# Performance work log

Hardware: AMD Instinct MI355X
Metric: run time of the kernel (lower is better)

## Reference

```python
import jax, jax.numpy as jnp
import numpy as np

N = 4096   # out_features (rows of W)
M = 4096   # in_features (cols of W)
S_L = 2048 # Givens pairs on rows
S_R = 2048 # Givens pairs on cols
T = 8192   # tokens (batch*seq)
EPS = 1e-6


def _disjoint_pairs(key, n_feat, n_pairs):
    perm = jax.random.permutation(key, n_feat)[: 2 * n_pairs]
    return perm.reshape(n_pairs, 2).astype(jnp.int32)


def setup_inputs() -> dict:
    key = jax.random.key(0)
    ks = jax.random.split(key, 8)
    x = jax.random.normal(ks[0], (T, M), dtype=jnp.float32)
    W = 0.02 * jax.random.normal(ks[1], (N, M), dtype=jnp.float32)
    bias = jnp.zeros((N,), dtype=jnp.float32)
    theta_L = 0.002 * jax.random.normal(ks[2], (S_L,), dtype=jnp.float32)
    theta_R = 0.002 * jax.random.normal(ks[3], (S_R,), dtype=jnp.float32)
    pairs_L = _disjoint_pairs(ks[4], N, S_L)
    pairs_R = _disjoint_pairs(ks[5], M, S_R)
    ecd_log_mag = jnp.zeros((N,), dtype=jnp.float32)
    base_row_norms = jnp.linalg.norm(W, axis=1)  # [N], captured at init
    return {"x": x, "W": W, "bias": bias, "theta_L": theta_L,
            "theta_R": theta_R, "ecd_log_mag": ecd_log_mag,
            "base_row_norms": base_row_norms, "pairs_L": pairs_L,
            "pairs_R": pairs_R}


def _rotate_rows(Wm, pairs, theta):
    # Disjoint Givens rotations on rows: gather pair rows, 2x2 rotate, scatter.
    i, j = pairs[:, 0], pairs[:, 1]
    c = jnp.cos(theta)[:, None]
    s = jnp.sin(theta)[:, None]
    ri, rj = Wm[i], Wm[j]              # [S, M] gathers
    return Wm.at[i].set(c * ri - s * rj).at[j].set(s * ri + c * rj)


def _rotate_cols(Wm, pairs, theta):
    i, j = pairs[:, 0], pairs[:, 1]
    c = jnp.cos(theta)[None, :]
    s = jnp.sin(theta)[None, :]
    ci, cj = Wm[:, i], Wm[:, j]        # [N, S] gathers
    return Wm.at[:, i].set(c * ci - s * cj).at[:, j].set(s * ci + c * cj)


def reference(x, W, bias, theta_L, theta_R, ecd_log_mag, base_row_norms,
              pairs_L, pairs_R):
    # Effective weight: W_eff = G_L(theta_L) @ W @ G_R(theta_R)^T
    W_eff = _rotate_rows(_rotate_cols(W, pairs_R, theta_R), pairs_L, theta_L)
    # Magnitude (ECD) rescaling: restore base per-row norms modulated by
    # learned log-magnitudes.
    row_norms = jnp.sqrt(jnp.sum(W_eff * W_eff, axis=1) + EPS)  # [N]
    scale = base_row_norms * jnp.exp(ecd_log_mag) / row_norms   # [N]
    W_eff = W_eff * scale[:, None]
    return x @ W_eff.T + bias
```

## Files before the change

kernel.cpp:

```cpp
#include <hip/hip_runtime.h>
#include <cstdint>
#include <cstddef>

constexpr int T_N = 8192;
constexpr int MM  = 4096;
constexpr int NN  = 4096;
constexpr int S_L = 2048;
constexpr int S_R = 2048;
constexpr float EPS_ = 1e-6f;

typedef float  f32x4   __attribute__((ext_vector_type(4)));
typedef __bf16 bf16x8  __attribute__((ext_vector_type(8)));
typedef unsigned short ushort8 __attribute__((ext_vector_type(8)));

__device__ __forceinline__ unsigned short f2bf(float f) {
  unsigned int u = __float_as_uint(f);
  u += 0x7FFFu + ((u >> 16) & 1u);
  return (unsigned short)(u >> 16);
}

__global__ void init_cols(float* colC, float* colS, int* colP) {
  int i = blockIdx.x * blockDim.x + threadIdx.x;
  if (i < MM) { colC[i] = 1.f; colS[i] = 0.f; colP[i] = i; }
}

__global__ void build_cols(const float* __restrict__ thR, const int* __restrict__ prR,
                           float* colC, float* colS, int* colP) {
  int s = blockIdx.x * blockDim.x + threadIdx.x;
  if (s < S_R) {
    int i = prR[2*s], j = prR[2*s+1];
    float c = cosf(thR[s]), sn = sinf(thR[s]);
    colC[i] = c; colS[i] = -sn; colP[i] = j;
    colC[j] = c; colS[j] =  sn; colP[j] = i;
  }
}

__global__ __launch_bounds__(256) void weff_pair(
    const float* __restrict__ W, const float* __restrict__ brn, const float* __restrict__ elm,
    const float* __restrict__ thL, const int* __restrict__ prL,
    const float* __restrict__ colC, const float* __restrict__ colS, const int* __restrict__ colP,
    unsigned short* __restrict__ Wb)
{
  __shared__ __align__(16) float rI[MM];
  __shared__ __align__(16) float rJ[MM];
  __shared__ float red[8];

  int s   = blockIdx.x;
  int tid = threadIdx.x;
  int i = prL[2*s], j = prL[2*s+1];
  float cl = cosf(thL[s]), sl = sinf(thL[s]);
  const float* Wi = W + (size_t)i * MM;
  const float* Wj = W + (size_t)j * MM;

  for (int m = tid * 4; m < MM; m += 1024) {
    *(f32x4*)&rI[m] = *(const f32x4*)&Wi[m];
    *(f32x4*)&rJ[m] = *(const f32x4*)&Wj[m];
  }
  __syncthreads();

  float ssi = 0.f, ssj = 0.f;
  for (int m = tid; m < MM; m += 256) {
    int p = colP[m];
    float c = colC[m], sn = colS[m];
    float vi = c * rI[m] + sn * rI[p];
    float vj = c * rJ[m] + sn * rJ[p];
    float ei = cl * vi - sl * vj;
    float ej = sl * vi + cl * vj;
    ssi += ei * ei;
    ssj += ej * ej;
  }
  #pragma unroll
  for (int o = 32; o; o >>= 1) { ssi += __shfl_xor(ssi, o); ssj += __shfl_xor(ssj, o); }
  int lane = tid & 63, wid = tid >> 6;
  if (lane == 0) { red[wid] = ssi; red[4 + wid] = ssj; }
  __syncthreads();
  float ti = red[0] + red[1] + red[2] + red[3];
  float tj = red[4] + red[5] + red[6] + red[7];
  float sci = brn[i] * expf(elm[i]) / sqrtf(ti + EPS_);
  float scj = brn[j] * expf(elm[j]) / sqrtf(tj + EPS_);

  for (int m0 = tid * 8; m0 < MM; m0 += 2048) {
    ushort8 pi, pj;
    #pragma unroll
    for (int q = 0; q < 8; q++) {
      int m = m0 + q;
      int p = colP[m];
      float c = colC[m], sn = colS[m];
      float vi = c * rI[m] + sn * rI[p];
      float vj = c * rJ[m] + sn * rJ[p];
      pi[q] = f2bf((cl * vi - sl * vj) * sci);
      pj[q] = f2bf((sl * vi + cl * vj) * scj);
    }
    *(ushort8*)&Wb[(size_t)i * MM + m0] = pi;
    *(ushort8*)&Wb[(size_t)j * MM + m0] = pj;
  }
}

__global__ __launch_bounds__(256) void conv_x(const float* __restrict__ x,
                                              unsigned short* __restrict__ xb) {
  const size_t total = (size_t)T_N * MM / 8;
  for (size_t i = (size_t)blockIdx.x * 256 + threadIdx.x; i < total; i += 2048ull * 256ull) {
    const float* s = x + i * 8;
    f32x4 v0 = *(const f32x4*)s;
    f32x4 v1 = *(const f32x4*)(s + 4);
    ushort8 p;
    p[0] = f2bf(v0.x); p[1] = f2bf(v0.y); p[2] = f2bf(v0.z); p[3] = f2bf(v0.w);
    p[4] = f2bf(v1.x); p[5] = f2bf(v1.y); p[6] = f2bf(v1.z); p[7] = f2bf(v1.w);
    *(ushort8*)(xb + i * 8) = p;
  }
}

typedef const __attribute__((address_space(1))) unsigned int* as1_u32p;
typedef __attribute__((address_space(3))) unsigned int* as3_u32p;

__device__ __forceinline__ void gl_lds16(const void* g, void* l) {
  __builtin_amdgcn_global_load_lds((as1_u32p)g, (as3_u32p)l, 16, 0, 0);
}

constexpr int GBM = 256, GBN = 256, GBK = 64;
constexpr int NTK = MM / GBK;
constexpr int BUFB = GBM * GBK * 2;

#define SB0() __builtin_amdgcn_sched_barrier(0)
#define BAR() __builtin_amdgcn_s_barrier()
#define LGKM(N) do { asm volatile("s_waitcnt lgkmcnt(" #N ")" ::: "memory"); \
                     SB0(); } while (0)

#define RD_A8(DST, AB, MIH)                                                   \
  _Pragma("unroll") for (int i_ = 0; i_ < 4; ++i_)                            \
  _Pragma("unroll") for (int k_ = 0; k_ < 2; ++k_)                            \
    DST[i_][k_] = *(const bf16x8*)((AB) + arow0 + ((MIH) * 4 + i_) * 2048     \
                                    + ((k_ * 64 + lg * 16) ^ sw));

#define RD_B4(DST, BB, NIH)                                                   \
  _Pragma("unroll") for (int n_ = 0; n_ < 2; ++n_)                            \
  _Pragma("unroll") for (int k_ = 0; k_ < 2; ++k_)                            \
    DST[n_][k_] = *(const bf16x8*)((BB) + brow0 + ((NIH) * 2 + n_) * 2048     \
                                    + ((k_ * 64 + lg * 16) ^ sw));

#define QMF(AF, BF, MI0, NI0)                                                 \
  __builtin_amdgcn_s_setprio(1);                                              \
  _Pragma("unroll") for (int k_ = 0; k_ < 2; ++k_)                            \
  _Pragma("unroll") for (int i_ = 0; i_ < 4; ++i_)                            \
  _Pragma("unroll") for (int n_ = 0; n_ < 2; ++n_)                            \
    acc[(MI0) + i_][(NI0) + n_] = __builtin_amdgcn_mfma_f32_16x16x32_bf16(    \
        AF[i_][k_], BF[n_][k_], acc[(MI0) + i_][(NI0) + n_], 0, 0, 0);        \
  __builtin_amdgcn_s_setprio(0);

#define STG_A(KOF, BUF, H)                                                    \
  _Pragma("unroll") for (int l_ = 2 * (H); l_ < 2 * (H) + 2; ++l_)            \
    gl_lds16(sA + (size_t)l_ * (64 * MM) + (KOF),                             \
             ldsA + (BUF) * BUFB + dstb + l_ * 8192);
#define STG_B(KOF, BUF, H)                                                    \
  _Pragma("unroll") for (int l_ = 2 * (H); l_ < 2 * (H) + 2; ++l_)            \
    gl_lds16(sB + (size_t)l_ * (64 * MM) + (KOF),                             \
             ldsB + (BUF) * BUFB + dstb + l_ * 8192);

#define GATE6  asm volatile("s_waitcnt vmcnt(6)" ::: "memory")
#define GATE0v asm volatile("s_waitcnt vmcnt(0)" ::: "memory")
#define GNONE  do { } while (0)

#define TILE8(T, BB, DOB1, DOA2, GATEK)                                       \
  {                                                                           \
    const char* Ab_ = ldsA + (BB) * BUFB;                                     \
    const char* Bb_ = ldsB + (BB) * BUFB;                                     \
    bf16x8 afA[4][2], afB[4][2], bfA[2][2], bfB[2][2];                        \
           \
    RD_A8(afA, Ab_, 0);                                                       \
    RD_B4(bfA, Bb_, 0);                                                       \
    if (DOB1) { STG_B(((T) + 1) * GBK, (BB) ^ 1, 1); }                        \
    LGKM(8);                                                                  \
    BAR();                                                                    \
    LGKM(0);                                                                  \
    QMF(afA, bfA, 0, 0);                                                      \
    BAR();                                                                    \
                                         \
    RD_A8(afB, Ab_, 1);                                                       \
    BAR();                                                                    \
    LGKM(0);                                                                  \
    QMF(afB, bfA, 4, 0);                                                      \
    BAR();                                                                    \
                          \
    RD_B4(bfB, Bb_, 1);                                                       \
    if (DOA2) { STG_A(((T) + 2) * GBK, (BB), 0); }                            \
    BAR();                                                                    \
    LGKM(0);                                                                  \
    QMF(afB, bfB, 4, 2);                                                      \
    BAR();                                                                    \
               \
    if (DOA2) { STG_A(((T) + 2) * GBK, (BB), 1);                              \
                STG_B(((T) + 2) * GBK, (BB), 0); }                            \
    GATEK;                                                                    \
    BAR();                                                                    \
    QMF(afA, bfB, 0, 2);                                                      \
    BAR();                                                                    \
  }

__global__ __launch_bounds__(512, 2) void gemm8(
    const unsigned short* __restrict__ xb,
    const unsigned short* __restrict__ wb,
    const float* __restrict__ bias,
    float* __restrict__ C)
{
  __shared__ __align__(16) unsigned short As[2 * GBM * GBK];
  __shared__ __align__(16) unsigned short Bs[2 * GBN * GBK];
  char* ldsA = (char*)As;
  char* ldsB = (char*)Bs;

  int bid = blockIdx.x;
  int swz = (bid & 7) * 64 + (bid >> 3);
  int tn = swz & 15, tm = swz >> 4;
  const int trow0 = tm * GBM;
  const int tcol0 = tn * GBN;

  int tid  = threadIdx.x;
  int lane = tid & 63;
  int wid  = tid >> 6;
  int wr = wid >> 2, wc = wid & 3;
  int lr = lane & 15;
  int lg = lane >> 4;
  const int sw = (lr & 7) << 4;
  const int arow0 = (wr * 128 + lr) * 128;
  const int brow0 = (wc * 64  + lr) * 128;

  const int r0   = tid >> 3;
  const int colg = (tid & 7) ^ (r0 & 7);
  const unsigned short* sA = xb + (size_t)(trow0 + r0) * MM + colg * 8;
  const unsigned short* sB = wb + (size_t)(tcol0 + r0) * MM + colg * 8;
  const int dstb = tid * 16;

  f32x4 acc[8][4];
  #pragma unroll
  for (int i = 0; i < 8; i++)
    #pragma unroll
    for (int j = 0; j < 4; j++) {
      f32x4 z = {0.f, 0.f, 0.f, 0.f};
      acc[i][j] = z;
    }

  STG_A(0, 0, 0); STG_A(0, 0, 1); STG_B(0, 0, 0); STG_B(0, 0, 1);
  STG_A(GBK, 1, 0); STG_A(GBK, 1, 1); STG_B(GBK, 1, 0);
  asm volatile("s_waitcnt vmcnt(6)" ::: "memory");
  __builtin_amdgcn_s_barrier();

  #pragma unroll 1
  for (int t = 0; t < NTK - 2; t += 2) {
    TILE8(t,     0, 1, 1, GATE6);
    TILE8(t + 1, 1, 1, 1, GATE6);
  }
  TILE8(NTK - 2, 0, 1, 0, GATE0v);
  TILE8(NTK - 1, 1, 0, 0, GNONE);

  #pragma unroll
  for (int ni = 0; ni < 4; ++ni) {
    int col = tcol0 + wc * 64 + ni * 16 + lr;
    float bi = bias[col];
    #pragma unroll
    for (int mi = 0; mi < 8; ++mi) {
      int rr0 = trow0 + wr * 128 + mi * 16 + lg * 4;
      #pragma unroll
      for (int qq = 0; qq < 4; ++qq)
        C[(size_t)(rr0 + qq) * NN + col] = acc[mi][ni][qq] + bi;
    }
  }
}

constexpr int BM = 128, BN = 128, BK = 64;

__global__ __launch_bounds__(256) void gemm_fb(
    const float* __restrict__ xf,
    const unsigned short* __restrict__ wb, const float* __restrict__ bias,
    float* __restrict__ C)
{
  __shared__ __align__(16) unsigned short As2[BM * BK];
  __shared__ __align__(16) unsigned short Bs2[BN * BK];

  int bid = blockIdx.x;
  int swz = (bid & 7) * 256 + (bid >> 3);
  int tn = swz & 31;
  int tm = swz >> 5;

  int tid  = threadIdx.x;
  int lane = tid & 63;
  int wid  = tid >> 6;
  int wr = wid >> 1, wc = wid & 1;
  int lr = lane & 15;
  int lg = lane >> 4;

  f32x4 acc[4][4];
  #pragma unroll
  for (int i = 0; i < 4; i++)
    #pragma unroll
    for (int j = 0; j < 4; j++) {
      f32x4 z = {0.f, 0.f, 0.f, 0.f};
      acc[i][j] = z;
    }

  int srow = tid >> 3;
  int scol = (tid & 7) * 8;
  const size_t a_base = (size_t)(tm * BM) * MM;
  const size_t b_base = (size_t)(tn * BN) * MM;

  for (int k0 = 0; k0 < MM; k0 += BK) {
    #pragma unroll
    for (int c = 0; c < 4; c++) {
      int row = c * 32 + srow;
      gl_lds16(wb + b_base + (size_t)row * MM + k0 + scol,
               (char*)Bs2 + (c * 256 + wid * 64) * 16);
    }
    #pragma unroll
    for (int c = 0; c < 4; c++) {
      int row = c * 32 + srow;
      const float* s = xf + a_base + (size_t)row * MM + k0 + scol;
      f32x4 v0 = *(const f32x4*)s;
      f32x4 v1 = *(const f32x4*)(s + 4);
      ushort8 p;
      p[0] = f2bf(v0.x); p[1] = f2bf(v0.y); p[2] = f2bf(v0.z); p[3] = f2bf(v0.w);
      p[4] = f2bf(v1.x); p[5] = f2bf(v1.y); p[6] = f2bf(v1.z); p[7] = f2bf(v1.w);
      *(ushort8*)&As2[(c * 256 + tid) * 8] = p;
    }
    __syncthreads();

    #pragma unroll
    for (int kk = 0; kk < 2; kk++) {
      bf16x8 a[4], b[4];
      #pragma unroll
      for (int i = 0; i < 4; i++) {
        a[i] = *(const bf16x8*)&As2[(wr * 64 + i * 16 + lr) * BK + kk * 32 + lg * 8];
        b[i] = *(const bf16x8*)&Bs2[(wc * 64 + i * 16 + lr) * BK + kk * 32 + lg * 8];
      }
      #pragma unroll
      for (int i = 0; i < 4; i++)
        #pragma unroll
        for (int j = 0; j < 4; j++)
          acc[i][j] = __builtin_amdgcn_mfma_f32_16x16x32_bf16(a[i], b[j], acc[i][j], 0, 0, 0);
    }
    __syncthreads();
  }

  int gn0 = tn * BN + wc * 64;
  int gt0 = tm * BM + wr * 64;
  #pragma unroll
  for (int j = 0; j < 4; j++) {
    int gn = gn0 + j * 16 + lr;
    float bi = bias[gn];
    #pragma unroll
    for (int i = 0; i < 4; i++) {
      int t0 = gt0 + i * 16 + lg * 4;
      #pragma unroll
      for (int q = 0; q < 4; q++)
        C[(size_t)(t0 + q) * NN + gn] = acc[i][j][q] + bi;
    }
  }
}

extern "C" void kernel_launch(void* const* d_in, const int* in_sizes, int n_in,
                              void* d_out, int out_size, void* d_ws, size_t ws_size,
                              hipStream_t stream)
{
  const float* x    = (const float*)d_in[0];
  const float* W    = (const float*)d_in[1];
  const float* bias = (const float*)d_in[2];
  const float* thL  = (const float*)d_in[3];
  const float* thR  = (const float*)d_in[4];
  const float* elm  = (const float*)d_in[5];
  const float* brn  = (const float*)d_in[6];
  const int*   prL  = (const int*)d_in[7];
  const int*   prR  = (const int*)d_in[8];
  float* out = (float*)d_out;

  char* ws = (char*)d_ws;
  unsigned short* Wb = (unsigned short*)ws;
  size_t off = (size_t)NN * MM * 2;
  float* colC = (float*)(ws + off); off += MM * 4;
  float* colS = (float*)(ws + off); off += MM * 4;
  int*   colP = (int*)  (ws + off); off += MM * 4;
  unsigned short* xb = (unsigned short*)(ws + off);
  bool use_xb = ws_size >= off + (size_t)T_N * MM * 2;

  init_cols <<<16, 256, 0, stream>>>(colC, colS, colP);
  build_cols<<< 8, 256, 0, stream>>>(thR, prR, colC, colS, colP);
  weff_pair <<<S_L, 256, 0, stream>>>(W, brn, elm, thL, prL, colC, colS, colP, Wb);

  if (use_xb) {
    conv_x<<<2048, 256, 0, stream>>>(x, xb);
    gemm8<<<512, 512, 0, stream>>>(xb, Wb, bias, out);
  } else {
    gemm_fb<<<2048, 256, 0, stream>>>(x, Wb, bias, out);
  }
}
```

Before: 320.4 us.

## Split LDS fragment reads by k-half and restructure MFMA phases, remap tile order

Fragment reads from LDS are now issued per k-half, so each MFMA group can start after a partial lgkmcnt wait instead of waiting for every load. The four compute phases are merged into three, with barriers placed before the waits, to cut barrier count and overlap LDS latency with MFMA work. Block-to-tile mapping is also changed so consecutive blocks walk along the M dimension first, which changes L2 reuse of the weight tiles. The partial-wait counts depend on the order in which loads are issued, so a mismatch could read fragments before they arrive.

```diff
diff --git a/kernel.cpp b/kernel.cpp
--- a/kernel.cpp
+++ b/kernel.cpp
@@ -126,25 +126,22 @@
 #define LGKM(N) do { asm volatile("s_waitcnt lgkmcnt(" #N ")" ::: "memory"); \
                      SB0(); } while (0)
 
-#define RD_A8(DST, AB, MIH)                                                   \
+#define RD_A4K(DST, AB, MIH, KK)                                              \
   _Pragma("unroll") for (int i_ = 0; i_ < 4; ++i_)                            \
-  _Pragma("unroll") for (int k_ = 0; k_ < 2; ++k_)                            \
-    DST[i_][k_] = *(const bf16x8*)((AB) + arow0 + ((MIH) * 4 + i_) * 2048     \
-                                    + ((k_ * 64 + lg * 16) ^ sw));
-
-#define RD_B4(DST, BB, NIH)                                                   \
+    DST[i_][KK] = *(const bf16x8*)((AB) + arow0 + ((MIH) * 4 + i_) * 2048     \
+                                    + (((KK) * 64 + lg * 16) ^ sw));
+
+#define RD_B2K(DST, BB, NIH, KK)                                              \
   _Pragma("unroll") for (int n_ = 0; n_ < 2; ++n_)                            \
-  _Pragma("unroll") for (int k_ = 0; k_ < 2; ++k_)                            \
-    DST[n_][k_] = *(const bf16x8*)((BB) + brow0 + ((NIH) * 2 + n_) * 2048     \
-                                    + ((k_ * 64 + lg * 16) ^ sw));
-
-#define QMF(AF, BF, MI0, NI0)                                                 \
+    DST[n_][KK] = *(const bf16x8*)((BB) + brow0 + ((NIH) * 2 + n_) * 2048     \
+                                    + (((KK) * 64 + lg * 16) ^ sw));
+
+#define QMF8(AF, BF, MI0, NI0, KK)                                            \
   __builtin_amdgcn_s_setprio(1);                                              \
-  _Pragma("unroll") for (int k_ = 0; k_ < 2; ++k_)                            \
   _Pragma("unroll") for (int i_ = 0; i_ < 4; ++i_)                            \
   _Pragma("unroll") for (int n_ = 0; n_ < 2; ++n_)                            \
     acc[(MI0) + i_][(NI0) + n_] = __builtin_amdgcn_mfma_f32_16x16x32_bf16(    \
-        AF[i_][k_], BF[n_][k_], acc[(MI0) + i_][(NI0) + n_], 0, 0, 0);        \
+        AF[i_][KK], BF[n_][KK], acc[(MI0) + i_][(NI0) + n_], 0, 0, 0);        \
   __builtin_amdgcn_s_setprio(0);
 
 #define STG_A(KOF, BUF, H)                                                    \
@@ -160,39 +157,52 @@
 #define GATE0v asm volatile("s_waitcnt vmcnt(0)" ::: "memory")
 #define GNONE  do { } while (0)
 
-#define TILE8(T, BB, DOB1, DOA2, GATEK)                                       \
+#define TILE3(T, BB, DOB1, DOA2, GATEK)                                       \
   {                                                                           \
     const char* Ab_ = ldsA + (BB) * BUFB;                                     \
     const char* Bb_ = ldsB + (BB) * BUFB;                                     \
     bf16x8 afA[4][2], afB[4][2], bfA[2][2], bfB[2][2];                        \
-           \
-    RD_A8(afA, Ab_, 0);                                                       \
-    RD_B4(bfA, Bb_, 0);                                                       \
+                                         \
+    RD_B2K(bfA, Bb_, 0, 0);                                                   \
+    RD_A4K(afA, Ab_, 0, 0);                                                   \
+    SB0();                                                                    \
+    RD_B2K(bfA, Bb_, 0, 1);                                                   \
+    RD_A4K(afA, Ab_, 0, 1);                                                   \
+    SB0();                                                                    \
     if (DOB1) { STG_B(((T) + 1) * GBK, (BB) ^ 1, 1); }                        \
-    LGKM(8);                                                                  \
-    BAR();                                                                    \
+    BAR();                                                                    \
+    LGKM(6);                                                                  \
+    QMF8(afA, bfA, 0, 0, 0);                                                  \
     LGKM(0);                                                                  \
-    QMF(afA, bfA, 0, 0);                                                      \
+    QMF8(afA, bfA, 0, 0, 1);                                                  \
     BAR();                                                                    \
                                          \
-    RD_A8(afB, Ab_, 1);                                                       \
-    BAR();                                                                    \
+    RD_A4K(afB, Ab_, 1, 0);                                                   \
+    SB0();                                                                    \
+    RD_A4K(afB, Ab_, 1, 1);                                                   \
+    SB0();                                                                    \
+    if (DOA2) { STG_A(((T) + 2) * GBK, (BB), 0); }                            \
+    BAR();                                                                    \
+    LGKM(4);                                                                  \
+    QMF8(afB, bfA, 4, 0, 0);                                                  \
     LGKM(0);                                                                  \
-    QMF(afB, bfA, 4, 0);                                                      \
-    BAR();                                                                    \
-                          \
-    RD_B4(bfB, Bb_, 1);                                                       \
-    if (DOA2) { STG_A(((T) + 2) * GBK, (BB), 0); }                            \
-    BAR();                                                                    \
-    LGKM(0);                                                                  \
-    QMF(afB, bfB, 4, 2);                                                      \
-    BAR();                                                                    \
-               \
+    QMF8(afB, bfA, 4, 0, 1);                                                  \
+    BAR();                                                                    \
+                     \
+    RD_B2K(bfB, Bb_, 1, 0);                                                   \
+    SB0();                                                                    \
+    RD_B2K(bfB, Bb_, 1, 1);                                                   \
+    SB0();                                                                    \
     if (DOA2) { STG_A(((T) + 2) * GBK, (BB), 1);                              \
                 STG_B(((T) + 2) * GBK, (BB), 0); }                            \
     GATEK;                                                                    \
     BAR();                                                                    \
-    QMF(afA, bfB, 0, 2);                                                      \
+    LGKM(2);                                                                  \
+    QMF8(afB, bfB, 4, 2, 0);                                                  \
+    LGKM(0);                                                                  \
+    QMF8(afB, bfB, 4, 2, 1);                                                  \
+    QMF8(afA, bfB, 0, 2, 0);                                                  \
+    QMF8(afA, bfB, 0, 2, 1);                                                  \
     BAR();                                                                    \
   }
 
@@ -209,7 +219,7 @@
 
   int bid = blockIdx.x;
   int swz = (bid & 7) * 64 + (bid >> 3);
-  int tn = swz & 15, tm = swz >> 4;
+  int tm = swz & 31, tn = swz >> 5;
   const int trow0 = tm * GBM;
   const int tcol0 = tn * GBN;
 
@@ -245,11 +255,11 @@
 
   #pragma unroll 1
   for (int t = 0; t < NTK - 2; t += 2) {
-    TILE8(t,     0, 1, 1, GATE6);
-    TILE8(t + 1, 1, 1, 1, GATE6);
-  }
-  TILE8(NTK - 2, 0, 1, 0, GATE0v);
-  TILE8(NTK - 1, 1, 0, 0, GNONE);
+    TILE3(t,     0, 1, 1, GATE6);
+    TILE3(t + 1, 1, 1, 1, GATE6);
+  }
+  TILE3(NTK - 2, 0, 1, 0, GATE0v);
+  TILE3(NTK - 1, 1, 0, 0, GNONE);
 
   #pragma unroll
   for (int ni = 0; ni < 4; ++ni) {
```

New measurement: 318.1 us. No clear change (-0.7%).

## Fuse x bf16 conversion into weight-prep kernel and restage GEMM prefetch slots

Applied to the files above, without the earlier changes.

Merges the x-to-bf16 conversion into the weight-transform launch as extra blocks, so both memory-bound prep passes share one grid and overlap instead of running back to back, and one launch is removed. The GEMM tile macro is also restructured: the four global-to-LDS stage issues are spread across the four MFMA phases, each placed after a sched barrier, and the B fragment is read before A. This aims for smoother memory issue during compute. It changes scheduling around the waitcnt gates, which must still cover the moved loads.

```diff
diff --git a/kernel.cpp b/kernel.cpp
--- a/kernel.cpp
+++ b/kernel.cpp
@@ -35,18 +35,35 @@
   }
 }
 
-__global__ __launch_bounds__(256) void weff_pair(
+__global__ __launch_bounds__(256) void weff_conv(
     const float* __restrict__ W, const float* __restrict__ brn, const float* __restrict__ elm,
     const float* __restrict__ thL, const int* __restrict__ prL,
     const float* __restrict__ colC, const float* __restrict__ colS, const int* __restrict__ colP,
-    unsigned short* __restrict__ Wb)
+    unsigned short* __restrict__ Wb,
+    const float* __restrict__ x, unsigned short* __restrict__ xb)
 {
   __shared__ __align__(16) float rI[MM];
   __shared__ __align__(16) float rJ[MM];
   __shared__ float red[8];
 
-  int s   = blockIdx.x;
+  int bid = blockIdx.x;
   int tid = threadIdx.x;
+
+  if (bid >= S_L) {
+    const size_t total = (size_t)T_N * MM / 8;
+    for (size_t i = (size_t)(bid - S_L) * 256 + tid; i < total; i += 2048ull * 256ull) {
+      const float* s = x + i * 8;
+      f32x4 v0 = *(const f32x4*)s;
+      f32x4 v1 = *(const f32x4*)(s + 4);
+      ushort8 p;
+      p[0] = f2bf(v0.x); p[1] = f2bf(v0.y); p[2] = f2bf(v0.z); p[3] = f2bf(v0.w);
+      p[4] = f2bf(v1.x); p[5] = f2bf(v1.y); p[6] = f2bf(v1.z); p[7] = f2bf(v1.w);
+      *(ushort8*)(xb + i * 8) = p;
+    }
+    return;
+  }
+
+  int s = bid;
   int i = prL[2*s], j = prL[2*s+1];
   float cl = cosf(thL[s]), sl = sinf(thL[s]);
   const float* Wi = W + (size_t)i * MM;
@@ -96,20 +113,6 @@
   }
 }
 
-__global__ __launch_bounds__(256) void conv_x(const float* __restrict__ x,
-                                              unsigned short* __restrict__ xb) {
-  const size_t total = (size_t)T_N * MM / 8;
-  for (size_t i = (size_t)blockIdx.x * 256 + threadIdx.x; i < total; i += 2048ull * 256ull) {
-    const float* s = x + i * 8;
-    f32x4 v0 = *(const f32x4*)s;
-    f32x4 v1 = *(const f32x4*)(s + 4);
-    ushort8 p;
-    p[0] = f2bf(v0.x); p[1] = f2bf(v0.y); p[2] = f2bf(v0.z); p[3] = f2bf(v0.w);
-    p[4] = f2bf(v1.x); p[5] = f2bf(v1.y); p[6] = f2bf(v1.z); p[7] = f2bf(v1.w);
-    *(ushort8*)(xb + i * 8) = p;
-  }
-}
-
 typedef const __attribute__((address_space(1))) unsigned int* as1_u32p;
 typedef __attribute__((address_space(3))) unsigned int* as3_u32p;
 
@@ -159,40 +162,44 @@
 #define GATE6  asm volatile("s_waitcnt vmcnt(6)" ::: "memory")
 #define GATE0v asm volatile("s_waitcnt vmcnt(0)" ::: "memory")
 #define GNONE  do { } while (0)
-
-#define TILE8(T, BB, DOB1, DOA2, GATEK)                                       \
+#define NOST   do { } while (0)
+
+#define TILE4(T, BB, ST1, ST2, ST3, ST4, GATE)                                \
   {                                                                           \
     const char* Ab_ = ldsA + (BB) * BUFB;                                     \
     const char* Bb_ = ldsB + (BB) * BUFB;                                     \
-    bf16x8 afA[4][2], afB[4][2], bfA[2][2], bfB[2][2];                        \
-           \
-    RD_A8(afA, Ab_, 0);                                                       \
-    RD_B4(bfA, Bb_, 0);                                                       \
-    if (DOB1) { STG_B(((T) + 1) * GBK, (BB) ^ 1, 1); }                        \
+    bf16x8 a0[4][2], a1[4][2], b0[2][2], b1[2][2];                            \
+                          \
+    RD_B4(b0, Bb_, 0);                                                        \
+    RD_A8(a0, Ab_, 0);                                                        \
+    SB0();                                                                    \
+    ST1;                                                                      \
     LGKM(8);                                                                  \
     BAR();                                                                    \
     LGKM(0);                                                                  \
-    QMF(afA, bfA, 0, 0);                                                      \
-    BAR();                                                                    \
-                                         \
-    RD_A8(afB, Ab_, 1);                                                       \
+    QMF(a0, b0, 0, 0);                                                        \
+    BAR();                                                                    \
+                                    \
+    RD_A8(a1, Ab_, 1);                                                        \
+    SB0();                                                                    \
+    ST2;                                                                      \
     BAR();                                                                    \
     LGKM(0);                                                                  \
-    QMF(afB, bfA, 4, 0);                                                      \
-    BAR();                                                                    \
-                          \
-    RD_B4(bfB, Bb_, 1);                                                       \
-    if (DOA2) { STG_A(((T) + 2) * GBK, (BB), 0); }                            \
+    QMF(a1, b0, 4, 0);                                                        \
+    BAR();                                                                    \
+                                    \
+    RD_B4(b1, Bb_, 1);                                                        \
+    SB0();                                                                    \
+    ST3;                                                                      \
     BAR();                                                                    \
     LGKM(0);                                                                  \
-    QMF(afB, bfB, 4, 2);                                                      \
-    BAR();                                                                    \
-               \
-    if (DOA2) { STG_A(((T) + 2) * GBK, (BB), 1);                              \
-                STG_B(((T) + 2) * GBK, (BB), 0); }                            \
-    GATEK;                                                                    \
-    BAR();                                                                    \
-    QMF(afA, bfB, 0, 2);                                                      \
+    QMF(a1, b1, 4, 2);                                                        \
+    BAR();                                                                    \
+                  \
+    ST4;                                                                      \
+    GATE;                                                                     \
+    BAR();                                                                    \
+    QMF(a0, b1, 0, 2);                                                        \
     BAR();                                                                    \
   }
 
@@ -245,11 +252,23 @@
 
   #pragma unroll 1
   for (int t = 0; t < NTK - 2; t += 2) {
-    TILE8(t,     0, 1, 1, GATE6);
-    TILE8(t + 1, 1, 1, 1, GATE6);
-  }
-  TILE8(NTK - 2, 0, 1, 0, GATE0v);
-  TILE8(NTK - 1, 1, 0, 0, GNONE);
+    TILE4(t, 0,
+          STG_B((t + 1) * GBK, 1, 1),
+          STG_A((t + 2) * GBK, 0, 0),
+          STG_A((t + 2) * GBK, 0, 1),
+          STG_B((t + 2) * GBK, 0, 0),
+          GATE6);
+    TILE4(t + 1, 1,
+          STG_B((t + 2) * GBK, 0, 1),
+          STG_A((t + 3) * GBK, 1, 0),
+          STG_A((t + 3) * GBK, 1, 1),
+          STG_B((t + 3) * GBK, 1, 0),
+          GATE6);
+  }
+  TILE4(NTK - 2, 0,
+        STG_B((NTK - 1) * GBK, 1, 1),
+        NOST, NOST, NOST, GATE0v);
+  TILE4(NTK - 1, 1, NOST, NOST, NOST, NOST, GNONE);
 
   #pragma unroll
   for (int ni = 0; ni < 4; ++ni) {
@@ -380,12 +399,14 @@
 
   init_cols <<<16, 256, 0, stream>>>(colC, colS, colP);
   build_cols<<< 8, 256, 0, stream>>>(thR, prR, colC, colS, colP);
-  weff_pair <<<S_L, 256, 0, stream>>>(W, brn, elm, thL, prL, colC, colS, colP, Wb);
 
   if (use_xb) {
-    conv_x<<<2048, 256, 0, stream>>>(x, xb);
+    weff_conv<<<S_L + 2048, 256, 0, stream>>>(W, brn, elm, thL, prL,
+                                              colC, colS, colP, Wb, x, xb);
     gemm8<<<512, 512, 0, stream>>>(xb, Wb, bias, out);
   } else {
+    weff_conv<<<S_L, 256, 0, stream>>>(W, brn, elm, thL, prL,
+                                       colC, colS, colP, Wb, x, xb);
     gemm_fb<<<2048, 256, 0, stream>>>(x, Wb, bias, out);
   }
 }
```

New measurement: 302.0 us, median of 2. -5.7%, faster.
